# Kernel optimization log

Measured on AMD Instinct MI355X. Metric: run time of the kernel, lower is better.

Reference implementation:

```python
import jax, jax.numpy as jnp
import numpy as np

L, B, N, D, H, DH, DFF = 12, 4, 512, 768, 12, 64, 3072
SCALE = 1.0 / np.sqrt(DH).astype(np.float32)


def _ln(x, s, b):
    m = x.mean(-1, keepdims=True)
    v = ((x - m) ** 2).mean(-1, keepdims=True)
    return (x - m) * jax.lax.rsqrt(v + 1e-5) * s + b


def setup_inputs() -> dict:
    key = jax.random.key(0)
    ks = jax.random.split(key, 6)
    w = 0.02
    return {
        "x": jax.random.normal(ks[0], (B, N, D), jnp.float32),
        "ln1_s": jnp.ones((L, D), jnp.float32),
        "ln1_b": jnp.zeros((L, D), jnp.float32),
        "wqkv": jax.random.normal(ks[1], (L, D, 3 * H * DH), jnp.float32) * w,
        "wo": jax.random.normal(ks[2], (L, H * DH, D), jnp.float32) * w,
        "bo": jnp.zeros((L, D), jnp.float32),
        "ln2_s": jnp.ones((L, D), jnp.float32),
        "ln2_b": jnp.zeros((L, D), jnp.float32),
        "w1": jax.random.normal(ks[3], (L, D, DFF), jnp.float32) * w,
        "b1": jnp.zeros((L, DFF), jnp.float32),
        "w2": jax.random.normal(ks[4], (L, DFF, D), jnp.float32) * w,
        "b2": jnp.zeros((L, D), jnp.float32),
    }


def reference(x, ln1_s, ln1_b, wqkv, wo, bo, ln2_s, ln2_b, w1, b1, w2, b2):
    b, n, d = x.shape

    def layer(x, p):
        l1s, l1b, qkv_w, wo_, bo_, l2s, l2b, w1_, b1_, w2_, b2_ = p
        # --- pre-norm multi-head self-attention (softmax) ---
        h = _ln(x, l1s, l1b)
        qkv = h @ qkv_w                              # [b, n, 3*H*DH]
        q, k, v = jnp.split(qkv, 3, axis=-1)
        def heads(t):                                # [b, n, H*DH] -> [b, H, n, DH]
            return t.reshape(b, n, H, DH).transpose(0, 2, 1, 3)
        q, k, v = heads(q), heads(k), heads(v)
        scores = jnp.einsum("bhnd,bhmd->bhnm", q, k) * SCALE
        attn = jax.nn.softmax(scores, axis=-1)       # [b, H, n, n]
        o = jnp.einsum("bhnm,bhmd->bhnd", attn, v)
        o = o.transpose(0, 2, 1, 3).reshape(b, n, H * DH)
        x = x + (o @ wo_ + bo_)                      # residual 1 (dropout p=0)
        # --- pre-norm feed-forward (GELU, exact erf as in torch) ---
        h2 = _ln(x, l2s, l2b)
        ff = jax.nn.gelu(h2 @ w1_ + b1_, approximate=False) @ w2_ + b2_
        x = x + ff                                   # residual 2
        return x, attn

    out, weights = jax.lax.scan(
        layer, x, (ln1_s, ln1_b, wqkv, wo, bo, ln2_s, ln2_b, w1, b1, w2, b2)
    )
    return out, weights  # weights: [L, b, H, n, n], matching the per-layer list
```

## Files before the change

### kernel.cpp

```cpp
#include <hip/hip_runtime.h>
#include <hip/hip_bf16.h>

typedef __hip_bfloat16 bf16;
typedef float f32x4 __attribute__((ext_vector_type(4)));
typedef __bf16 b16x8 __attribute__((ext_vector_type(8)));

constexpr int Lc = 12, Bc = 4, Nc = 512, Dc = 768, Hc = 12, DHc = 64, DFFc = 3072;
constexpr int QKVc = 3 * Dc;
constexpr int Mrows = Bc * Nc;
constexpr float SCALE = 0.125f;

__device__ __forceinline__ bf16 f2b(float x) { return __float2bfloat16(x); }

__device__ __forceinline__ void mfma_bf16(f32x4& d, b16x8 a, b16x8 b) {
  d = __builtin_amdgcn_mfma_f32_16x16x32_bf16(a, b, d, 0, 0, 0);
}

__device__ __forceinline__ void gload16(const bf16* g, bf16* l) {
  __builtin_amdgcn_global_load_lds(
      (const __attribute__((address_space(1))) void*)g,
      (__attribute__((address_space(3))) void*)l, 16, 0, 0);
}

template <int BM, int BN, int WM, int WN, int MODE, int SPLITK = 1>
__global__ __launch_bounds__(256) void gemm_bt(
    const bf16* __restrict__ Abase, const bf16* __restrict__ Btbase,
    const float* __restrict__ bias, float* __restrict__ xres,
    bf16* __restrict__ outb_,
    int M, int N, int K, int lda, int ldb, int ldc) {
  constexpr int MI = WM / 16, NI = WN / 16;
  constexpr int NWN = BN / WN;
  const int tid = threadIdx.x;
  const int lane = tid & 63, wave = tid >> 6;
  const int wm = (wave / NWN) * WM, wn = (wave % NWN) * WN;
  const int tm0 = blockIdx.x * BM, tn0 = blockIdx.y * BN;
  const int z = blockIdx.z;

  const bf16* A = Abase;
  const bf16* Bt = Btbase;
  bf16* outb = outb_;

  const int Kslice = K / SPLITK;
  const int kbase = (SPLITK > 1) ? z * Kslice : 0;

  __shared__ __align__(16) bf16 As[2][BM * 32];
  __shared__ __align__(16) bf16 Bs[2][BN * 32];

  f32x4 acc[MI][NI] = {};

  const int nt = Kslice >> 5;

  auto stage = [&](int buf, int k0) {
    #pragma unroll
    for (int rr = 0; rr < BM / 64; rr++) {
      int e = rr * 2048 + tid * 8;
      int r = e >> 5, kk = e & 31;
      gload16(A + (size_t)(tm0 + r) * lda + (kbase + k0 + kk), &As[buf][e]);
    }
    #pragma unroll
    for (int rr = 0; rr < BN / 64; rr++) {
      int e = rr * 2048 + tid * 8;
      int r = e >> 5, kk = e & 31;
      gload16(Bt + (size_t)(tn0 + r) * ldb + (kbase + k0 + kk), &Bs[buf][e]);
    }
  };

  stage(0, 0);
  __syncthreads();

  int cur = 0;
  for (int kt = 0; kt < nt; kt++) {
    if (kt + 1 < nt) stage(cur ^ 1, (kt + 1) * 32);

    b16x8 af[MI], bfr[NI];
    #pragma unroll
    for (int i = 0; i < MI; i++)
      af[i] = *(const b16x8*)(&As[cur][(wm + i * 16 + (lane & 15)) * 32 + (lane >> 4) * 8]);
    #pragma unroll
    for (int j = 0; j < NI; j++)
      bfr[j] = *(const b16x8*)(&Bs[cur][(wn + j * 16 + (lane & 15)) * 32 + (lane >> 4) * 8]);
    #pragma unroll
    for (int i = 0; i < MI; i++)
      #pragma unroll
      for (int j = 0; j < NI; j++)
        mfma_bf16(acc[i][j], af[i], bfr[j]);

    __syncthreads();
    cur ^= 1;
  }

  const int r0 = (lane >> 4) * 4;
  const int c0 = lane & 15;
  #pragma unroll
  for (int i = 0; i < MI; i++) {
    #pragma unroll
    for (int j = 0; j < NI; j++) {
      #pragma unroll
      for (int r = 0; r < 4; r++) {
        int row = tm0 + wm + i * 16 + r0 + r;
        int col = tn0 + wn + j * 16 + c0;
        float v = acc[i][j][r];
        if (MODE == 0) {
          outb[(size_t)row * ldc + col] = f2b(v);
        } else if (MODE == 1) {
          v += bias[col];
          float g = 0.5f * v * (1.0f + erff(v * 0.70710678118654752f));
          outb[(size_t)row * ldc + col] = f2b(g);
        } else if (MODE == 2) {
          if (SPLITK > 1) {
            if (z == 0) v += bias[col];
            atomicAdd(&xres[(size_t)row * ldc + col], v);
          } else {
            v += bias[col];
            xres[(size_t)row * ldc + col] += v;
          }
        }
      }
    }
  }
}

__global__ __launch_bounds__(256) void fattn_k(const bf16* __restrict__ qkv,
                                               const bf16* __restrict__ vt,
                                               float* __restrict__ attn_f,
                                               bf16* __restrict__ o) {
  const int bh = blockIdx.y;
  const int b = bh / Hc, h = bh % Hc;
  const int n0 = blockIdx.x * 32;
  const int tid = threadIdx.x, lane = tid & 63, wave = tid >> 6;
  const int wn = wave * 128;

  constexpr int KP = 72;
  __shared__ __align__(16) bf16 KV[512 * KP];
  __shared__ __align__(16) bf16 P[32 * 512];
  __shared__ float red[32][4];

  const bf16* qbase = qkv + (size_t)b * Nc * QKVc + h * DHc;
  const bf16* kbase = qbase + Dc;

  for (int e = tid * 8; e < 512 * 64; e += 2048) {
    int kv = e >> 6, c = e & 63;
    *(uint4*)(KV + kv * KP + c) = *(const uint4*)(kbase + (size_t)kv * QKVc + c);
  }
  b16x8 qf[2][2];
  #pragma unroll
  for (int ks = 0; ks < 2; ks++)
    #pragma unroll
    for (int i = 0; i < 2; i++)
      qf[ks][i] = *(const b16x8*)(qbase +
          (size_t)(n0 + i * 16 + (lane & 15)) * QKVc + ks * 32 + (lane >> 4) * 8);
  __syncthreads();

  f32x4 acc[2][8] = {};
  #pragma unroll
  for (int ks = 0; ks < 2; ks++) {
    #pragma unroll
    for (int j = 0; j < 8; j++) {
      b16x8 kf = *(const b16x8*)(KV + (wn + j * 16 + (lane & 15)) * KP +
                                 ks * 32 + (lane >> 4) * 8);
      #pragma unroll
      for (int i = 0; i < 2; i++)
        mfma_bf16(acc[i][j], qf[ks][i], kf);
    }
  }

  const bf16* vthead = vt + (size_t)bh * DHc * Nc;
  b16x8 vreg[16];
  #pragma unroll
  for (int r = 0; r < 16; r++)
    vreg[r] = *(const b16x8*)(vthead + r * 2048 + tid * 8);

  #pragma unroll
  for (int i = 0; i < 2; i++)
    #pragma unroll
    for (int j = 0; j < 8; j++)
      acc[i][j] *= SCALE;

  const int r0 = (lane >> 4) * 4, c0 = lane & 15;
  float rmax[2][4];
  #pragma unroll
  for (int i = 0; i < 2; i++)
    #pragma unroll
    for (int rr = 0; rr < 4; rr++) {
      float m = -1e30f;
      #pragma unroll
      for (int j = 0; j < 8; j++) m = fmaxf(m, acc[i][j][rr]);
      #pragma unroll
      for (int of = 1; of < 16; of <<= 1) m = fmaxf(m, __shfl_xor(m, of));
      rmax[i][rr] = m;
    }
  if (c0 == 0) {
    #pragma unroll
    for (int i = 0; i < 2; i++)
      #pragma unroll
      for (int rr = 0; rr < 4; rr++)
        red[i * 16 + r0 + rr][wave] = rmax[i][rr];
  }
  __syncthreads();
  #pragma unroll
  for (int i = 0; i < 2; i++)
    #pragma unroll
    for (int rr = 0; rr < 4; rr++) {
      int r = i * 16 + r0 + rr;
      rmax[i][rr] = fmaxf(fmaxf(red[r][0], red[r][1]), fmaxf(red[r][2], red[r][3]));
    }
  __syncthreads();

  float rsum[2][4];
  #pragma unroll
  for (int i = 0; i < 2; i++)
    #pragma unroll
    for (int rr = 0; rr < 4; rr++) {
      float s = 0.f;
      #pragma unroll
      for (int j = 0; j < 8; j++) {
        float e = expf(acc[i][j][rr] - rmax[i][rr]);
        acc[i][j][rr] = e;
        s += e;
      }
      #pragma unroll
      for (int of = 1; of < 16; of <<= 1) s += __shfl_xor(s, of);
      rsum[i][rr] = s;
    }
  if (c0 == 0) {
    #pragma unroll
    for (int i = 0; i < 2; i++)
      #pragma unroll
      for (int rr = 0; rr < 4; rr++)
        red[i * 16 + r0 + rr][wave] = rsum[i][rr];
  }
  __syncthreads();
  #pragma unroll
  for (int i = 0; i < 2; i++)
    #pragma unroll
    for (int rr = 0; rr < 4; rr++) {
      int r = i * 16 + r0 + rr;
      rsum[i][rr] = 1.0f / (red[r][0] + red[r][1] + red[r][2] + red[r][3]);
    }

  #pragma unroll
  for (int r = 0; r < 16; r++) {
    int d = r * 4 + wave;
    int kvs = (lane * 8) ^ ((d & 7) << 3);
    *(uint4*)(KV + d * 512 + kvs) = *(uint4*)&vreg[r];
  }

  float* of32 = attn_f + (size_t)bh * Nc * Nc;
  #pragma unroll
  for (int i = 0; i < 2; i++)
    #pragma unroll
    for (int j = 0; j < 8; j++)
      #pragma unroll
      for (int rr = 0; rr < 4; rr++) {
        int rloc = i * 16 + r0 + rr;
        int col = wn + j * 16 + c0;
        float p = acc[i][j][rr] * rsum[i][rr];
        of32[(size_t)(n0 + rloc) * Nc + col] = p;
        P[rloc * 512 + (col ^ ((rloc & 7) << 3))] = f2b(p);
      }
  __syncthreads();

  f32x4 oacc[2] = {};
  #pragma unroll
  for (int ks = 0; ks < 16; ks++) {
    int kvb = ks * 32 + ((lane >> 4) << 3);
    int dd = wave * 16 + (lane & 15);
    b16x8 bf_ = *(const b16x8*)(KV + dd * 512 + (kvb ^ ((dd & 7) << 3)));
    #pragma unroll
    for (int i = 0; i < 2; i++) {
      int q = i * 16 + (lane & 15);
      b16x8 af_ = *(const b16x8*)(P + q * 512 + (kvb ^ ((q & 7) << 3)));
      mfma_bf16(oacc[i], af_, bf_);
    }
  }
  #pragma unroll
  for (int i = 0; i < 2; i++)
    #pragma unroll
    for (int r = 0; r < 4; r++) {
      int row = b * Nc + n0 + i * 16 + r0 + r;
      o[(size_t)row * Dc + h * DHc + wave * 16 + c0] = f2b(oacc[i][r]);
    }
}

__global__ __launch_bounds__(256) void ln_k(const float* __restrict__ x,
                                            const float* __restrict__ s,
                                            const float* __restrict__ b,
                                            bf16* __restrict__ out) {
  const int row = blockIdx.x, tid = threadIdx.x;
  const float* xr = x + (size_t)row * Dc;
  float a0 = xr[tid], a1 = xr[tid + 256], a2 = xr[tid + 512];
  float sum = a0 + a1 + a2;
  float sq = a0 * a0 + a1 * a1 + a2 * a2;
  #pragma unroll
  for (int o = 32; o; o >>= 1) {
    sum += __shfl_down(sum, o);
    sq += __shfl_down(sq, o);
  }
  __shared__ float s1[4], s2[4];
  if ((tid & 63) == 0) { s1[tid >> 6] = sum; s2[tid >> 6] = sq; }
  __syncthreads();
  sum = s1[0] + s1[1] + s1[2] + s1[3];
  sq = s2[0] + s2[1] + s2[2] + s2[3];
  float m = sum * (1.0f / Dc);
  float var = sq * (1.0f / Dc) - m * m;
  float rs = rsqrtf(var + 1e-5f);
  bf16* orow = out + (size_t)row * Dc;
  orow[tid]       = f2b((a0 - m) * rs * s[tid]       + b[tid]);
  orow[tid + 256] = f2b((a1 - m) * rs * s[tid + 256] + b[tid + 256]);
  orow[tid + 512] = f2b((a2 - m) * rs * s[tid + 512] + b[tid + 512]);
}

__global__ __launch_bounds__(256) void twb_all_k(
    const float* __restrict__ wqkv_l, const float* __restrict__ wo_l,
    const float* __restrict__ w1_l, const float* __restrict__ w2_l,
    bf16* __restrict__ wTq, bf16* __restrict__ wTo,
    bf16* __restrict__ wT1, bf16* __restrict__ wT2) {
  int f = blockIdx.x;
  const float* in;
  bf16* outp;
  int K, Nw, n0, k0;
  if (f < 432)       { in = wqkv_l; outp = wTq; K = Dc;   Nw = QKVc; n0 = (f % 36) * 64; k0 = (f / 36) * 64; }
  else if (f < 576)  { f -= 432;  in = wo_l; outp = wTo; K = Dc;   Nw = Dc;   n0 = (f % 12) * 64; k0 = (f / 12) * 64; }
  else if (f < 1152) { f -= 576;  in = w1_l; outp = wT1; K = Dc;   Nw = DFFc; n0 = (f % 48) * 64; k0 = (f / 48) * 64; }
  else               { f -= 1152; in = w2_l; outp = wT2; K = DFFc; Nw = Dc;   n0 = (f % 12) * 64; k0 = (f / 12) * 64; }

  __shared__ bf16 t[64][65];
  const int tx = threadIdx.x & 63, ty = threadIdx.x >> 6;
  #pragma unroll
  for (int kk = ty; kk < 64; kk += 4)
    t[tx][kk] = f2b(in[(size_t)(k0 + kk) * Nw + n0 + tx]);
  __syncthreads();
  #pragma unroll
  for (int nn = ty; nn < 64; nn += 4)
    outp[(size_t)(n0 + nn) * K + k0 + tx] = t[nn][tx];
}

__global__ __launch_bounds__(256) void vtrans_k(const bf16* __restrict__ qkv,
                                                bf16* __restrict__ vt) {
  const int bh = blockIdx.z;
  const int b = bh / Hc, h = bh % Hc;
  const int n0 = blockIdx.x * 64;
  const bf16* src = qkv + (size_t)b * Nc * QKVc + 2 * Dc + h * DHc;
  __shared__ bf16 t[64][65];
  const int tx = threadIdx.x & 63, ty = threadIdx.x >> 6;
  #pragma unroll
  for (int nn = ty; nn < 64; nn += 4)
    t[tx][nn] = src[(size_t)(n0 + nn) * QKVc + tx];
  __syncthreads();
  bf16* dst = vt + (size_t)bh * DHc * Nc;
  #pragma unroll
  for (int dd = ty; dd < 64; dd += 4)
    dst[(size_t)dd * Nc + n0 + tx] = t[dd][tx];
}

extern "C" void kernel_launch(void* const* d_in, const int* in_sizes, int n_in,
                              void* d_out, int out_size, void* d_ws, size_t ws_size,
                              hipStream_t stream) {
  const float* x_in  = (const float*)d_in[0];
  const float* ln1_s = (const float*)d_in[1];
  const float* ln1_b = (const float*)d_in[2];
  const float* wqkv  = (const float*)d_in[3];
  const float* wo    = (const float*)d_in[4];
  const float* bo    = (const float*)d_in[5];
  const float* ln2_s = (const float*)d_in[6];
  const float* ln2_b = (const float*)d_in[7];
  const float* w1    = (const float*)d_in[8];
  const float* b1    = (const float*)d_in[9];
  const float* w2    = (const float*)d_in[10];
  const float* b2    = (const float*)d_in[11];
  float* out = (float*)d_out;

  char* ws = (char*)d_ws;
  float* x      = (float*)(ws + 0);
  bf16* h       = (bf16*)(ws + 6291456);
  bf16* qkv     = (bf16*)(ws + 9437184);
  bf16* o       = (bf16*)(ws + 18874368);
  bf16* ff      = (bf16*)(ws + 22020096);
  bf16* vt      = (bf16*)(ws + 34603008);
  bf16* wTq     = (bf16*)(ws + 37748736);
  bf16* wTo     = (bf16*)(ws + 41287680);
  bf16* wT1     = (bf16*)(ws + 42467328);
  bf16* wT2     = (bf16*)(ws + 47185920);
  if (ws_size < (size_t)51904512) return;

  hipMemcpyAsync(x, x_in, (size_t)Mrows * Dc * sizeof(float),
                 hipMemcpyDeviceToDevice, stream);

  constexpr size_t ATTN_BASE = (size_t)Mrows * Dc;
  constexpr size_t ATTN_L = (size_t)Bc * Hc * Nc * Nc;

  for (int l = 0; l < Lc; l++) {
    float* attn_l = out + ATTN_BASE + (size_t)l * ATTN_L;

    twb_all_k<<<1728, 256, 0, stream>>>(
        wqkv + (size_t)l * Dc * QKVc, wo + (size_t)l * Dc * Dc,
        w1 + (size_t)l * Dc * DFFc, w2 + (size_t)l * DFFc * Dc,
        wTq, wTo, wT1, wT2);

    ln_k<<<Mrows, 256, 0, stream>>>(x, ln1_s + l * Dc, ln1_b + l * Dc, h);
    gemm_bt<128, 128, 64, 64, 0><<<dim3(Mrows / 128, QKVc / 128, 1), 256, 0, stream>>>(
        h, wTq, nullptr, nullptr, qkv, Mrows, QKVc, Dc, Dc, Dc, QKVc);
    vtrans_k<<<dim3(Nc / 64, 1, Bc * Hc), 256, 0, stream>>>(qkv, vt);
    fattn_k<<<dim3(Nc / 32, Bc * Hc), 256, 0, stream>>>(qkv, vt, attn_l, o);
    gemm_bt<128, 64, 64, 32, 2, 2><<<dim3(Mrows / 128, Dc / 64, 2), 256, 0, stream>>>(
        o, wTo, bo + l * Dc, x, nullptr, Mrows, Dc, Dc, Dc, Dc, Dc);

    ln_k<<<Mrows, 256, 0, stream>>>(x, ln2_s + l * Dc, ln2_b + l * Dc, h);
    gemm_bt<128, 128, 64, 64, 1><<<dim3(Mrows / 128, DFFc / 128, 1), 256, 0, stream>>>(
        h, wT1, b1 + l * DFFc, nullptr, ff, Mrows, DFFc, Dc, Dc, Dc, DFFc);
    gemm_bt<128, 64, 64, 32, 2, 4><<<dim3(Mrows / 128, Dc / 64, 4), 256, 0, stream>>>(
        ff, wT2, b2 + l * Dc, x, nullptr, Mrows, Dc, DFFc, DFFc, DFFc, Dc);
  }

  hipMemcpyAsync(out, x, (size_t)Mrows * Dc * sizeof(float),
                 hipMemcpyDeviceToDevice, stream);
}
```

Measured before the change: 2.138 ms.

## Widen GEMM K-tile to 64 with XOR swizzle, fuse LN/weight-cast and V transpose

The GEMM now stages 64-wide K tiles, twice as deep as before, into LDS using an XOR-swizzled column layout. This halves the number of barrier iterations and avoids LDS bank conflicts on the fragment reads. The QKV GEMM epilogue also writes V transposed directly, which removes the separate vtrans kernel. The first LayerNorm is merged with the weight transpose/cast kernel into one launch. In exchange, the V transpose becomes strided scalar global stores, and the doubled LDS per block may reduce occupancy.

```diff
diff --git a/kernel.cpp b/kernel.cpp
--- a/kernel.cpp
+++ b/kernel.cpp
@@ -26,7 +26,7 @@
 __global__ __launch_bounds__(256) void gemm_bt(
     const bf16* __restrict__ Abase, const bf16* __restrict__ Btbase,
     const float* __restrict__ bias, float* __restrict__ xres,
-    bf16* __restrict__ outb_,
+    bf16* __restrict__ outb, bf16* __restrict__ vtout,
     int M, int N, int K, int lda, int ldb, int ldc) {
   constexpr int MI = WM / 16, NI = WN / 16;
   constexpr int NWN = BN / WN;
@@ -38,30 +38,31 @@
 
   const bf16* A = Abase;
   const bf16* Bt = Btbase;
-  bf16* outb = outb_;
 
   const int Kslice = K / SPLITK;
   const int kbase = (SPLITK > 1) ? z * Kslice : 0;
 
-  __shared__ __align__(16) bf16 As[2][BM * 32];
-  __shared__ __align__(16) bf16 Bs[2][BN * 32];
+  __shared__ __align__(16) bf16 As[2][BM * 64];
+  __shared__ __align__(16) bf16 Bs[2][BN * 64];
 
   f32x4 acc[MI][NI] = {};
 
-  const int nt = Kslice >> 5;
+  const int nt = Kslice >> 6;
 
   auto stage = [&](int buf, int k0) {
     #pragma unroll
-    for (int rr = 0; rr < BM / 64; rr++) {
-      int e = rr * 2048 + tid * 8;
-      int r = e >> 5, kk = e & 31;
-      gload16(A + (size_t)(tm0 + r) * lda + (kbase + k0 + kk), &As[buf][e]);
-    }
-    #pragma unroll
-    for (int rr = 0; rr < BN / 64; rr++) {
-      int e = rr * 2048 + tid * 8;
-      int r = e >> 5, kk = e & 31;
-      gload16(Bt + (size_t)(tn0 + r) * ldb + (kbase + k0 + kk), &Bs[buf][e]);
+    for (int rr = 0; rr < BM / 32; rr++) {
+      int idx = rr * 256 + tid;
+      int row = idx >> 3, c8 = idx & 7;
+      int sc = ((c8 ^ (row & 7)) << 3);
+      gload16(A + (size_t)(tm0 + row) * lda + (kbase + k0 + sc), &As[buf][idx * 8]);
+    }
+    #pragma unroll
+    for (int rr = 0; rr < BN / 32; rr++) {
+      int idx = rr * 256 + tid;
+      int row = idx >> 3, c8 = idx & 7;
+      int sc = ((c8 ^ (row & 7)) << 3);
+      gload16(Bt + (size_t)(tn0 + row) * ldb + (kbase + k0 + sc), &Bs[buf][idx * 8]);
     }
   };
 
@@ -70,20 +71,31 @@
 
   int cur = 0;
   for (int kt = 0; kt < nt; kt++) {
-    if (kt + 1 < nt) stage(cur ^ 1, (kt + 1) * 32);
-
-    b16x8 af[MI], bfr[NI];
-    #pragma unroll
-    for (int i = 0; i < MI; i++)
-      af[i] = *(const b16x8*)(&As[cur][(wm + i * 16 + (lane & 15)) * 32 + (lane >> 4) * 8]);
-    #pragma unroll
-    for (int j = 0; j < NI; j++)
-      bfr[j] = *(const b16x8*)(&Bs[cur][(wn + j * 16 + (lane & 15)) * 32 + (lane >> 4) * 8]);
-    #pragma unroll
-    for (int i = 0; i < MI; i++)
-      #pragma unroll
-      for (int j = 0; j < NI; j++)
-        mfma_bf16(acc[i][j], af[i], bfr[j]);
+    if (kt + 1 < nt) stage(cur ^ 1, (kt + 1) * 64);
+
+    b16x8 af[2][MI], bfr[2][NI];
+    #pragma unroll
+    for (int ks = 0; ks < 2; ks++) {
+      #pragma unroll
+      for (int i = 0; i < MI; i++) {
+        int r = wm + i * 16 + (lane & 15);
+        int c = ks * 4 + (lane >> 4);
+        af[ks][i] = *(const b16x8*)(&As[cur][r * 64 + ((c ^ (r & 7)) << 3)]);
+      }
+      #pragma unroll
+      for (int j = 0; j < NI; j++) {
+        int r = wn + j * 16 + (lane & 15);
+        int c = ks * 4 + (lane >> 4);
+        bfr[ks][j] = *(const b16x8*)(&Bs[cur][r * 64 + ((c ^ (r & 7)) << 3)]);
+      }
+    }
+    #pragma unroll
+    for (int ks = 0; ks < 2; ks++)
+      #pragma unroll
+      for (int i = 0; i < MI; i++)
+        #pragma unroll
+        for (int j = 0; j < NI; j++)
+          mfma_bf16(acc[i][j], af[ks][i], bfr[ks][j]);
 
     __syncthreads();
     cur ^= 1;
@@ -101,7 +113,13 @@
         int col = tn0 + wn + j * 16 + c0;
         float v = acc[i][j][r];
         if (MODE == 0) {
-          outb[(size_t)row * ldc + col] = f2b(v);
+          bf16 bv = f2b(v);
+          outb[(size_t)row * ldc + col] = bv;
+          if (col >= 2 * Dc) {
+            int cv = col - 2 * Dc;
+            int bh = (row >> 9) * Hc + (cv >> 6);
+            vtout[((size_t)bh * DHc + (cv & 63)) * Nc + (row & 511)] = bv;
+          }
         } else if (MODE == 1) {
           v += bias[col];
           float g = 0.5f * v * (1.0f + erff(v * 0.70710678118654752f));
@@ -282,6 +300,59 @@
     }
 }
 
+__global__ __launch_bounds__(256) void lntwb_k(
+    const float* __restrict__ x, const float* __restrict__ s,
+    const float* __restrict__ b, bf16* __restrict__ out,
+    const float* __restrict__ wqkv_l, const float* __restrict__ wo_l,
+    const float* __restrict__ w1_l, const float* __restrict__ w2_l,
+    bf16* __restrict__ wTq, bf16* __restrict__ wTo,
+    bf16* __restrict__ wT1, bf16* __restrict__ wT2) {
+  __shared__ bf16 t[64][65];
+  const int tid = threadIdx.x;
+  if (blockIdx.x < 2048) {
+    const int row = blockIdx.x;
+    const float* xr = x + (size_t)row * Dc;
+    float a0 = xr[tid], a1 = xr[tid + 256], a2 = xr[tid + 512];
+    float sum = a0 + a1 + a2;
+    float sq = a0 * a0 + a1 * a1 + a2 * a2;
+    #pragma unroll
+    for (int o = 32; o; o >>= 1) {
+      sum += __shfl_down(sum, o);
+      sq += __shfl_down(sq, o);
+    }
+    float* s1 = (float*)t;
+    float* s2 = s1 + 4;
+    if ((tid & 63) == 0) { s1[tid >> 6] = sum; s2[tid >> 6] = sq; }
+    __syncthreads();
+    sum = s1[0] + s1[1] + s1[2] + s1[3];
+    sq = s2[0] + s2[1] + s2[2] + s2[3];
+    float m = sum * (1.0f / Dc);
+    float var = sq * (1.0f / Dc) - m * m;
+    float rs = rsqrtf(var + 1e-5f);
+    bf16* orow = out + (size_t)row * Dc;
+    orow[tid]       = f2b((a0 - m) * rs * s[tid]       + b[tid]);
+    orow[tid + 256] = f2b((a1 - m) * rs * s[tid + 256] + b[tid + 256]);
+    orow[tid + 512] = f2b((a2 - m) * rs * s[tid + 512] + b[tid + 512]);
+    return;
+  }
+  int f = blockIdx.x - 2048;
+  const float* in;
+  bf16* outp;
+  int K, Nw, n0, k0;
+  if (f < 432)       { in = wqkv_l; outp = wTq; K = Dc;   Nw = QKVc; n0 = (f % 36) * 64; k0 = (f / 36) * 64; }
+  else if (f < 576)  { f -= 432;  in = wo_l; outp = wTo; K = Dc;   Nw = Dc;   n0 = (f % 12) * 64; k0 = (f / 12) * 64; }
+  else if (f < 1152) { f -= 576;  in = w1_l; outp = wT1; K = Dc;   Nw = DFFc; n0 = (f % 48) * 64; k0 = (f / 48) * 64; }
+  else               { f -= 1152; in = w2_l; outp = wT2; K = DFFc; Nw = Dc;   n0 = (f % 12) * 64; k0 = (f / 12) * 64; }
+  const int tx = tid & 63, ty = tid >> 6;
+  #pragma unroll
+  for (int kk = ty; kk < 64; kk += 4)
+    t[tx][kk] = f2b(in[(size_t)(k0 + kk) * Nw + n0 + tx]);
+  __syncthreads();
+  #pragma unroll
+  for (int nn = ty; nn < 64; nn += 4)
+    outp[(size_t)(n0 + nn) * K + k0 + tx] = t[nn][tx];
+}
+
 __global__ __launch_bounds__(256) void ln_k(const float* __restrict__ x,
                                             const float* __restrict__ s,
                                             const float* __restrict__ b,
@@ -308,49 +379,6 @@
   orow[tid]       = f2b((a0 - m) * rs * s[tid]       + b[tid]);
   orow[tid + 256] = f2b((a1 - m) * rs * s[tid + 256] + b[tid + 256]);
   orow[tid + 512] = f2b((a2 - m) * rs * s[tid + 512] + b[tid + 512]);
-}
-
-__global__ __launch_bounds__(256) void twb_all_k(
-    const float* __restrict__ wqkv_l, const float* __restrict__ wo_l,
-    const float* __restrict__ w1_l, const float* __restrict__ w2_l,
-    bf16* __restrict__ wTq, bf16* __restrict__ wTo,
-    bf16* __restrict__ wT1, bf16* __restrict__ wT2) {
-  int f = blockIdx.x;
-  const float* in;
-  bf16* outp;
-  int K, Nw, n0, k0;
-  if (f < 432)       { in = wqkv_l; outp = wTq; K = Dc;   Nw = QKVc; n0 = (f % 36) * 64; k0 = (f / 36) * 64; }
-  else if (f < 576)  { f -= 432;  in = wo_l; outp = wTo; K = Dc;   Nw = Dc;   n0 = (f % 12) * 64; k0 = (f / 12) * 64; }
-  else if (f < 1152) { f -= 576;  in = w1_l; outp = wT1; K = Dc;   Nw = DFFc; n0 = (f % 48) * 64; k0 = (f / 48) * 64; }
-  else               { f -= 1152; in = w2_l; outp = wT2; K = DFFc; Nw = Dc;   n0 = (f % 12) * 64; k0 = (f / 12) * 64; }
-
-  __shared__ bf16 t[64][65];
-  const int tx = threadIdx.x & 63, ty = threadIdx.x >> 6;
-  #pragma unroll
-  for (int kk = ty; kk < 64; kk += 4)
-    t[tx][kk] = f2b(in[(size_t)(k0 + kk) * Nw + n0 + tx]);
-  __syncthreads();
-  #pragma unroll
-  for (int nn = ty; nn < 64; nn += 4)
-    outp[(size_t)(n0 + nn) * K + k0 + tx] = t[nn][tx];
-}
-
-__global__ __launch_bounds__(256) void vtrans_k(const bf16* __restrict__ qkv,
-                                                bf16* __restrict__ vt) {
-  const int bh = blockIdx.z;
-  const int b = bh / Hc, h = bh % Hc;
-  const int n0 = blockIdx.x * 64;
-  const bf16* src = qkv + (size_t)b * Nc * QKVc + 2 * Dc + h * DHc;
-  __shared__ bf16 t[64][65];
-  const int tx = threadIdx.x & 63, ty = threadIdx.x >> 6;
-  #pragma unroll
-  for (int nn = ty; nn < 64; nn += 4)
-    t[tx][nn] = src[(size_t)(n0 + nn) * QKVc + tx];
-  __syncthreads();
-  bf16* dst = vt + (size_t)bh * DHc * Nc;
-  #pragma unroll
-  for (int dd = ty; dd < 64; dd += 4)
-    dst[(size_t)dd * Nc + n0 + tx] = t[dd][tx];
 }
 
 extern "C" void kernel_launch(void* const* d_in, const int* in_sizes, int n_in,
@@ -392,24 +420,23 @@
   for (int l = 0; l < Lc; l++) {
     float* attn_l = out + ATTN_BASE + (size_t)l * ATTN_L;
 
-    twb_all_k<<<1728, 256, 0, stream>>>(
+    lntwb_k<<<3776, 256, 0, stream>>>(
+        x, ln1_s + l * Dc, ln1_b + l * Dc, h,
         wqkv + (size_t)l * Dc * QKVc, wo + (size_t)l * Dc * Dc,
         w1 + (size_t)l * Dc * DFFc, w2 + (size_t)l * DFFc * Dc,
         wTq, wTo, wT1, wT2);
 
-    ln_k<<<Mrows, 256, 0, stream>>>(x, ln1_s + l * Dc, ln1_b + l * Dc, h);
     gemm_bt<128, 128, 64, 64, 0><<<dim3(Mrows / 128, QKVc / 128, 1), 256, 0, stream>>>(
-        h, wTq, nullptr, nullptr, qkv, Mrows, QKVc, Dc, Dc, Dc, QKVc);
-    vtrans_k<<<dim3(Nc / 64, 1, Bc * Hc), 256, 0, stream>>>(qkv, vt);
+        h, wTq, nullptr, nullptr, qkv, vt, Mrows, QKVc, Dc, Dc, Dc, QKVc);
     fattn_k<<<dim3(Nc / 32, Bc * Hc), 256, 0, stream>>>(qkv, vt, attn_l, o);
     gemm_bt<128, 64, 64, 32, 2, 2><<<dim3(Mrows / 128, Dc / 64, 2), 256, 0, stream>>>(
-        o, wTo, bo + l * Dc, x, nullptr, Mrows, Dc, Dc, Dc, Dc, Dc);
+        o, wTo, bo + l * Dc, x, nullptr, nullptr, Mrows, Dc, Dc, Dc, Dc, Dc);
 
     ln_k<<<Mrows, 256, 0, stream>>>(x, ln2_s + l * Dc, ln2_b + l * Dc, h);
     gemm_bt<128, 128, 64, 64, 1><<<dim3(Mrows / 128, DFFc / 128, 1), 256, 0, stream>>>(
-        h, wT1, b1 + l * DFFc, nullptr, ff, Mrows, DFFc, Dc, Dc, Dc, DFFc);
+        h, wT1, b1 + l * DFFc, nullptr, ff, nullptr, Mrows, DFFc, Dc, Dc, Dc, DFFc);
     gemm_bt<128, 64, 64, 32, 2, 4><<<dim3(Mrows / 128, Dc / 64, 4), 256, 0, stream>>>(
-        ff, wT2, b2 + l * Dc, x, nullptr, Mrows, Dc, DFFc, DFFc, DFFc, Dc);
+        ff, wT2, b2 + l * Dc, x, nullptr, nullptr, Mrows, Dc, DFFc, DFFc, DFFc, Dc);
   }
 
   hipMemcpyAsync(out, x, (size_t)Mrows * Dc * sizeof(float),
```

Measured after the change: 1.996 ms. 6.6% less time.
